# Kernel optimization log

Hardware: AMD Instinct MI355X
Metric: run time of the kernel (lower is better)

## Reference

```python
import jax, jax.numpy as jnp
import numpy as np

SIGMA = 1.0
EPS = 1e-8  # torch nn.CosineSimilarity eps


def setup_inputs() -> dict:
    key = jax.random.key(0)
    kx, ky = jax.random.split(key)
    ex = jax.random.normal(kx, (8192, 768), dtype=jnp.float32)
    ey = jax.random.normal(ky, (16384, 768), dtype=jnp.float32)
    return {"ex": ex, "ey": ey}


def _halfnormal_log_prob(v, sigma):
    # HalfNormal(sigma).log_prob(v) = 0.5*log(2/pi) - log(sigma) - v^2/(2 sigma^2)
    logc = 0.5 * jnp.log(jnp.asarray(2.0 / np.pi, v.dtype)) - jnp.log(jnp.asarray(sigma, v.dtype))
    return logc - v * v / (2.0 * sigma * sigma)


def reference(ex, ey):
    Nx, Ny = ex.shape[0], ey.shape[0]
    # cosine similarity matrix [Nx, Ny]; norms clamped like torch CosineSimilarity
    nx = jnp.maximum(jnp.linalg.norm(ex, axis=-1), EPS)  # [Nx]
    ny = jnp.maximum(jnp.linalg.norm(ey, axis=-1), EPS)  # [Ny]
    sims = jnp.einsum('nd,md->nm', ex, ey) / (nx[:, None] * ny[None, :])
    # dim = argmax([Nx, Ny]); Nx < Ny here -> reduce over axis 1 (ey side)
    dim = int(np.argmax([Nx, Ny]))
    C = sims.max(axis=dim)  # length min(Nx, Ny)
    x = 1.0 - C[:Nx]
    y = 1.0 - C[:Ny]
    lx = _halfnormal_log_prob(x, SIGMA)
    ly = _halfnormal_log_prob(y, SIGMA)
    return ((-jnp.exp(lx) * lx).sum(), (-jnp.exp(ly) * ly).sum())
```

## Files before the change

kernel.cpp:

```cpp
#include <hip/hip_runtime.h>
#include <cstdint>

#define D_DIM 768
#define BM 128
#define BN 256
#define BK 64
#define NT 12
#define ABYTES (BM * BK)
#define SLOT   (BM * BK + BN * BK)

typedef int   intx8    __attribute__((ext_vector_type(8)));
typedef float floatx16 __attribute__((ext_vector_type(16)));

#define SCALE_ONE 0x7F7F7F7F


__device__ inline void lds_load16(const void* g, void* lds) {
  __builtin_amdgcn_global_load_lds(
      (const __attribute__((address_space(1))) unsigned int*)g,
      (__attribute__((address_space(3))) unsigned int*)lds,
      16, 0, 0);
}

__device__ inline intx8 ldfrag(const unsigned char* p, int o0, int o1) {
  intx8 r;
  *(int4*)&r       = *(const int4*)(p + o0);
  *((int4*)&r + 1) = *(const int4*)(p + o1);
  return r;
}


__global__ __launch_bounds__(256) void norm_cast_kernel(
    const float* __restrict__ EX, const float* __restrict__ EY,
    unsigned int* __restrict__ XO, unsigned int* __restrict__ YO, int Nx) {
  int row = blockIdx.x * 4 + (threadIdx.x >> 6);
  int lane = threadIdx.x & 63;
  const float* X = (row < Nx) ? EX : EY;
  unsigned int* Y = (row < Nx) ? XO : YO;
  int r = (row < Nx) ? row : (row - Nx);
  const float4* xr = (const float4*)(X + (size_t)r * D_DIM);
  float4 a = xr[lane];
  float4 b = xr[lane + 64];
  float4 c = xr[lane + 128];
  float ss = a.x*a.x + a.y*a.y + a.z*a.z + a.w*a.w
           + b.x*b.x + b.y*b.y + b.z*b.z + b.w*b.w
           + c.x*c.x + c.y*c.y + c.z*c.z + c.w*c.w;
  #pragma unroll
  for (int off = 32; off > 0; off >>= 1) ss += __shfl_xor(ss, off, 64);
  float s = 1.0f / fmaxf(sqrtf(ss), 1e-8f);
  unsigned int* yr = Y + (size_t)r * (D_DIM / 4);
  int d;
  d = __builtin_amdgcn_cvt_pk_fp8_f32(a.x * s, a.y * s, 0, false);
  d = __builtin_amdgcn_cvt_pk_fp8_f32(a.z * s, a.w * s, d, true);
  yr[lane] = (unsigned int)d;
  d = __builtin_amdgcn_cvt_pk_fp8_f32(b.x * s, b.y * s, 0, false);
  d = __builtin_amdgcn_cvt_pk_fp8_f32(b.z * s, b.w * s, d, true);
  yr[lane + 64] = (unsigned int)d;
  d = __builtin_amdgcn_cvt_pk_fp8_f32(c.x * s, c.y * s, 0, false);
  d = __builtin_amdgcn_cvt_pk_fp8_f32(c.z * s, c.w * s, d, true);
  yr[lane + 128] = (unsigned int)d;
}


#define STAGE(SL, KO) do {                                                     \
    unsigned char* dst_ = lds + (SL) * SLOT;                                   \
    lds_load16(gA + (KO),            dst_ + wave * 2048);                      \
    lds_load16(gA + (KO) + g16,      dst_ + wave * 2048 + 1024);               \
    lds_load16(gB + (KO),            dst_ + ABYTES + wave * 4096);             \
    lds_load16(gB + (KO) + g16,      dst_ + ABYTES + wave * 4096 + 1024);      \
    lds_load16(gB + (KO) + 2 * g16,  dst_ + ABYTES + wave * 4096 + 2048);      \
    lds_load16(gB + (KO) + 3 * g16,  dst_ + ABYTES + wave * 4096 + 3072);      \
  } while (0)

#define MFMA(d, va, vb)                                                        \
  d = __builtin_amdgcn_mfma_scale_f32_32x32x64_f8f6f4(                         \
      va, vb, d, 0, 0, 0, SCALE_ONE, 0, SCALE_ONE)

#define COMPUTE(SL) do {                                                       \
    const unsigned char* buf_ = lds + (SL) * SLOT;                             \
    intx8 a0 = ldfrag(buf_ + arow,        o0, o1);                             \
    intx8 a1 = ldfrag(buf_ + arow + 2048, o0, o1);                             \
    intx8 b;                                                                   \
    __builtin_amdgcn_s_setprio(1);                                             \
    b = ldfrag(buf_ + brow, o0, o1);                                           \
    MFMA(acc[0][0], a0, b);                                                    \
    MFMA(acc[1][0], a1, b);                                                    \
    b = ldfrag(buf_ + brow + 2048, o0, o1);                                    \
    MFMA(acc[0][1], a0, b);                                                    \
    MFMA(acc[1][1], a1, b);                                                    \
    b = ldfrag(buf_ + brow + 4096, o0, o1);                                    \
    MFMA(acc[0][2], a0, b);                                                    \
    MFMA(acc[1][2], a1, b);                                                    \
    b = ldfrag(buf_ + brow + 6144, o0, o1);                                    \
    MFMA(acc[0][3], a0, b);                                                    \
    MFMA(acc[1][3], a1, b);                                                    \
    __builtin_amdgcn_s_setprio(0);                                             \
  } while (0)

#define WAITB(VMC) do {                                                        \
    asm volatile("s_waitcnt vmcnt(" #VMC ")" ::: "memory");                    \
    __builtin_amdgcn_s_barrier();                                              \
  } while (0)

__global__ __launch_bounds__(256, 2) void gemm_max_kernel(
    const unsigned char* __restrict__ A,
    const unsigned char* __restrict__ B,
    float* __restrict__ partial,
    int Nx) {
  __shared__ unsigned char lds[3 * SLOT];
  __shared__ float red[2][BM];

  const int tid  = threadIdx.x;
  const int wave = tid >> 6;
  const int lane = tid & 63;
  const int wm = wave >> 1;
  const int wn = wave & 1;
  const int l31 = lane & 31;
  const int h   = lane >> 5;

  const int lid    = blockIdx.y * gridDim.x + blockIdx.x;
  const int xcd    = lid & 7;
  const int idx    = lid >> 3;
  const int sgrp   = idx >> 6;
  const int within = idx & 63;
  const int bx = sgrp * 8 + (within & 7);
  const int by = xcd * 8 + (within >> 3);

  const int bm0 = bx * BM;
  const int bn0 = by * BN;

  floatx16 acc[2][4];
  #pragma unroll
  for (int mt = 0; mt < 2; ++mt)
    #pragma unroll
    for (int nt = 0; nt < 4; ++nt)
      acc[mt][nt] = (floatx16)(0.f);

  const int akey = l31 & 3;
  const int o0 = ((2 * h + 0) ^ akey) * 16;
  const int o1 = ((2 * h + 1) ^ akey) * 16;
  const int arow = (wm * 64 + l31) * 64;
  const int brow = ABYTES + (wn * 128 + l31) * 64;

  const int srow = lane >> 2;
  const int sj = (lane & 3) ^ (srow & 3);
  const unsigned char* gA = A + (size_t)(bm0 + wave * 32 + srow) * D_DIM + sj * 16;
  const unsigned char* gB = B + (size_t)(bn0 + wave * 64 + srow) * D_DIM + sj * 16;
  const size_t g16 = (size_t)16 * D_DIM;

  STAGE(0, 0);
  STAGE(1, BK);

  #pragma unroll 1
  for (int t0 = 0; t0 < 9; t0 += 3) {
    const int kb = t0 * BK;
    WAITB(6); STAGE(2, kb + 2 * BK); COMPUTE(0);
    WAITB(6); STAGE(0, kb + 3 * BK); COMPUTE(1);
    WAITB(6); STAGE(1, kb + 4 * BK); COMPUTE(2);
  }
  WAITB(6); STAGE(2, 11 * BK); COMPUTE(0);
  WAITB(6);                    COMPUTE(1);
  WAITB(0);                    COMPUTE(2);

  #pragma unroll
  for (int mt = 0; mt < 2; ++mt) {
    #pragma unroll
    for (int reg = 0; reg < 16; ++reg) {
      float v = fmaxf(fmaxf(acc[mt][0][reg], acc[mt][1][reg]),
                      fmaxf(acc[mt][2][reg], acc[mt][3][reg]));
      #pragma unroll
      for (int off = 1; off < 32; off <<= 1)
        v = fmaxf(v, __shfl_xor(v, off, 64));
      if (l31 == 0) {
        int r = wm * 64 + mt * 32 + (reg & 3) + 8 * (reg >> 2) + 4 * h;
        red[wn][r] = v;
      }
    }
  }
  __syncthreads();
  if (tid < BM) {
    float m = fmaxf(red[0][tid], red[1][tid]);
    partial[(size_t)by * Nx + bm0 + tid] = m;
  }
}


__global__ __launch_bounds__(256) void rowmax_kernel(
    const float* __restrict__ partial, float* __restrict__ bsum, int Nx, int ncb) {
  __shared__ float sdata[4];
  int r = blockIdx.x * blockDim.x + threadIdx.x;
  float m = -1e30f;
  for (int cb = 0; cb < ncb; ++cb)
    m = fmaxf(m, partial[(size_t)cb * Nx + r]);
  float x = 1.0f - m;
  const float logc = -0.22579135264472744f;
  float l = logc - 0.5f * x * x;
  float t = -__expf(l) * l;
  #pragma unroll
  for (int off = 32; off > 0; off >>= 1) t += __shfl_xor(t, off, 64);
  int wave = threadIdx.x >> 6;
  int lane = threadIdx.x & 63;
  if (lane == 0) sdata[wave] = t;
  __syncthreads();
  if (threadIdx.x == 0)
    bsum[blockIdx.x] = sdata[0] + sdata[1] + sdata[2] + sdata[3];
}


__global__ __launch_bounds__(64) void final_kernel(
    const float* __restrict__ bsum, float* __restrict__ out, int nb) {
  int lane = threadIdx.x;
  float s = (lane < nb) ? bsum[lane] : 0.f;
  #pragma unroll
  for (int off = 32; off > 0; off >>= 1) s += __shfl_xor(s, off, 64);
  if (lane == 0) { out[0] = s; out[1] = s; }
}


extern "C" void kernel_launch(void* const* d_in, const int* in_sizes, int n_in,
                              void* d_out, int out_size, void* d_ws, size_t ws_size,
                              hipStream_t stream) {
  const float* ex = (const float*)d_in[0];
  const float* ey = (const float*)d_in[1];
  const int Nx = in_sizes[0] / D_DIM;
  const int Ny = in_sizes[1] / D_DIM;
  const int ncb = Ny / BN;

  char* ws = (char*)d_ws;
  unsigned char* exn = (unsigned char*)ws;
  unsigned char* eyn = exn + (size_t)Nx * D_DIM;
  float* partial = (float*)(ws + (size_t)(Nx + Ny) * D_DIM);
  float* bsum    = partial + (size_t)ncb * Nx;

  norm_cast_kernel<<<(Nx + Ny) / 4, 256, 0, stream>>>(
      ex, ey, (unsigned int*)exn, (unsigned int*)eyn, Nx);
  gemm_max_kernel<<<dim3(Nx / BM, Ny / BN), 256, 0, stream>>>(exn, eyn, partial, Nx);
  rowmax_kernel<<<Nx / 256, 256, 0, stream>>>(partial, bsum, Nx, ncb);
  final_kernel<<<1, 64, 0, stream>>>(bsum, (float*)d_out, Nx / 256);
}
```

Measured before the change: 280.8 us.

## Switch GEMM to double-buffered LDS with new swizzle and fuse final reduction

The GEMM main loop moves from a three-slot LDS ring with explicit vmcnt waits and s_setprio hints to a two-slot ping-pong with a full __syncthreads per stage. It also uses a new XOR swizzle for LDS staging and fragment reads, and a 1D launch grid. The separate final reduction kernel is removed, and rowmax blocks atomically add their partial sums straight into the output. This cuts prefetch depth and LDS use and drops one launch. The atomics assume the output starts at zero, and the shallower pipeline may expose more memory latency.

Result: slower. 362.0 us (+28.9%).

```diff
diff --git a/kernel.cpp b/kernel.cpp
--- a/kernel.cpp
+++ b/kernel.cpp
@@ -5,9 +5,11 @@
 #define BM 128
 #define BN 256
 #define BK 64
-#define NT 12
-#define ABYTES (BM * BK)
-#define SLOT   (BM * BK + BN * BK)
+#define ASZ (BM * BK)
+#define BSZ (BN * BK)
+#define SLOT (ASZ + BSZ)
+#define NBX 64
+#define NBY 64
 
 typedef int   intx8    __attribute__((ext_vector_type(8)));
 typedef float floatx16 __attribute__((ext_vector_type(16)));
@@ -62,52 +64,48 @@
 }
 
 
-#define STAGE(SL, KO) do {                                                     \
-    unsigned char* dst_ = lds + (SL) * SLOT;                                   \
-    lds_load16(gA + (KO),            dst_ + wave * 2048);                      \
-    lds_load16(gA + (KO) + g16,      dst_ + wave * 2048 + 1024);               \
-    lds_load16(gB + (KO),            dst_ + ABYTES + wave * 4096);             \
-    lds_load16(gB + (KO) + g16,      dst_ + ABYTES + wave * 4096 + 1024);      \
-    lds_load16(gB + (KO) + 2 * g16,  dst_ + ABYTES + wave * 4096 + 2048);      \
-    lds_load16(gB + (KO) + 3 * g16,  dst_ + ABYTES + wave * 4096 + 3072);      \
+#define STAGE(P, KO) do {                                                      \
+    unsigned char* dst_ = lds + (P) * SLOT;                                    \
+    unsigned char* dA_ = dst_ + wave * 2048;                                   \
+    unsigned char* dB_ = dst_ + ASZ + wave * 4096;                             \
+    lds_load16(gA + (KO),            dA_);                                     \
+    lds_load16(gA + (KO) + g16,      dA_ + 1024);                              \
+    lds_load16(gB + (KO),            dB_);                                     \
+    lds_load16(gB + (KO) + g16,      dB_ + 1024);                              \
+    lds_load16(gB + (KO) + 2 * g16,  dB_ + 2048);                              \
+    lds_load16(gB + (KO) + 3 * g16,  dB_ + 3072);                              \
   } while (0)
 
 #define MFMA(d, va, vb)                                                        \
   d = __builtin_amdgcn_mfma_scale_f32_32x32x64_f8f6f4(                         \
       va, vb, d, 0, 0, 0, SCALE_ONE, 0, SCALE_ONE)
 
-#define COMPUTE(SL) do {                                                       \
-    const unsigned char* buf_ = lds + (SL) * SLOT;                             \
-    intx8 a0 = ldfrag(buf_ + arow,        o0, o1);                             \
-    intx8 a1 = ldfrag(buf_ + arow + 2048, o0, o1);                             \
+#define COMPUTE(P) do {                                                        \
+    const unsigned char* bA_ = lds + (P) * SLOT + wm * 4096;                   \
+    const unsigned char* bB_ = lds + (P) * SLOT + ASZ + wn * 8192;             \
+    intx8 a0 = ldfrag(bA_,        o0, o1);                                     \
+    intx8 a1 = ldfrag(bA_ + 2048, o0, o1);                                     \
     intx8 b;                                                                   \
-    __builtin_amdgcn_s_setprio(1);                                             \
-    b = ldfrag(buf_ + brow, o0, o1);                                           \
+    b = ldfrag(bB_, o0, o1);                                                   \
     MFMA(acc[0][0], a0, b);                                                    \
     MFMA(acc[1][0], a1, b);                                                    \
-    b = ldfrag(buf_ + brow + 2048, o0, o1);                                    \
+    b = ldfrag(bB_ + 2048, o0, o1);                                            \
     MFMA(acc[0][1], a0, b);                                                    \
     MFMA(acc[1][1], a1, b);                                                    \
-    b = ldfrag(buf_ + brow + 4096, o0, o1);                                    \
+    b = ldfrag(bB_ + 4096, o0, o1);                                            \
     MFMA(acc[0][2], a0, b);                                                    \
     MFMA(acc[1][2], a1, b);                                                    \
-    b = ldfrag(buf_ + brow + 6144, o0, o1);                                    \
+    b = ldfrag(bB_ + 6144, o0, o1);                                            \
     MFMA(acc[0][3], a0, b);                                                    \
     MFMA(acc[1][3], a1, b);                                                    \
-    __builtin_amdgcn_s_setprio(0);                                             \
   } while (0)
 
-#define WAITB(VMC) do {                                                        \
-    asm volatile("s_waitcnt vmcnt(" #VMC ")" ::: "memory");                    \
-    __builtin_amdgcn_s_barrier();                                              \
-  } while (0)
-
-__global__ __launch_bounds__(256, 2) void gemm_max_kernel(
+__global__ __launch_bounds__(256) void gemm_max_kernel(
     const unsigned char* __restrict__ A,
     const unsigned char* __restrict__ B,
     float* __restrict__ partial,
     int Nx) {
-  __shared__ unsigned char lds[3 * SLOT];
+  __shared__ unsigned char lds[2 * SLOT];
   __shared__ float red[2][BM];
 
   const int tid  = threadIdx.x;
@@ -118,7 +116,7 @@
   const int l31 = lane & 31;
   const int h   = lane >> 5;
 
-  const int lid    = blockIdx.y * gridDim.x + blockIdx.x;
+  const int lid    = blockIdx.x;
   const int xcd    = lid & 7;
   const int idx    = lid >> 3;
   const int sgrp   = idx >> 6;
@@ -136,31 +134,30 @@
     for (int nt = 0; nt < 4; ++nt)
       acc[mt][nt] = (floatx16)(0.f);
 
-  const int akey = l31 & 3;
-  const int o0 = ((2 * h + 0) ^ akey) * 16;
-  const int o1 = ((2 * h + 1) ^ akey) * 16;
-  const int arow = (wm * 64 + l31) * 64;
-  const int brow = ABYTES + (wn * 128 + l31) * 64;
-
-  const int srow = lane >> 2;
-  const int sj = (lane & 3) ^ (srow & 3);
-  const unsigned char* gA = A + (size_t)(bm0 + wave * 32 + srow) * D_DIM + sj * 16;
-  const unsigned char* gB = B + (size_t)(bn0 + wave * 64 + srow) * D_DIM + sj * 16;
+  const int key  = (l31 >> 1) & 7;
+  const int lrow = (l31 >> 1) * 128;
+  const int c0   = 2 * h;
+  const int o0 = lrow + ((((l31 & 1) << 2) | c0)       ^ key) * 16;
+  const int o1 = lrow + ((((l31 & 1) << 2) | (c0 + 1)) ^ key) * 16;
+
+  const int ls   = (lane & 7) ^ (lane >> 3);
+  const int srow = 2 * (lane >> 3) + (ls >> 2);
+  const int sc   = ls & 3;
+  const unsigned char* gA = A + (size_t)(bm0 + wave * 32 + srow) * D_DIM + sc * 16;
+  const unsigned char* gB = B + (size_t)(bn0 + wave * 64 + srow) * D_DIM + sc * 16;
   const size_t g16 = (size_t)16 * D_DIM;
 
   STAGE(0, 0);
-  STAGE(1, BK);
+  __syncthreads();
 
   #pragma unroll 1
-  for (int t0 = 0; t0 < 9; t0 += 3) {
-    const int kb = t0 * BK;
-    WAITB(6); STAGE(2, kb + 2 * BK); COMPUTE(0);
-    WAITB(6); STAGE(0, kb + 3 * BK); COMPUTE(1);
-    WAITB(6); STAGE(1, kb + 4 * BK); COMPUTE(2);
-  }
-  WAITB(6); STAGE(2, 11 * BK); COMPUTE(0);
-  WAITB(6);                    COMPUTE(1);
-  WAITB(0);                    COMPUTE(2);
+  for (int t2 = 0; t2 < 5; ++t2) {
+    const int kb = t2 * 2 * BK;
+    STAGE(1, kb + BK);     COMPUTE(0);  __syncthreads();
+    STAGE(0, kb + 2 * BK); COMPUTE(1);  __syncthreads();
+  }
+  STAGE(1, 11 * BK);  COMPUTE(0);  __syncthreads();
+  COMPUTE(1);
 
   #pragma unroll
   for (int mt = 0; mt < 2; ++mt) {
@@ -186,7 +183,7 @@
 
 
 __global__ __launch_bounds__(256) void rowmax_kernel(
-    const float* __restrict__ partial, float* __restrict__ bsum, int Nx, int ncb) {
+    const float* __restrict__ partial, float* __restrict__ out, int Nx, int ncb) {
   __shared__ float sdata[4];
   int r = blockIdx.x * blockDim.x + threadIdx.x;
   float m = -1e30f;
@@ -202,18 +199,11 @@
   int lane = threadIdx.x & 63;
   if (lane == 0) sdata[wave] = t;
   __syncthreads();
-  if (threadIdx.x == 0)
-    bsum[blockIdx.x] = sdata[0] + sdata[1] + sdata[2] + sdata[3];
-}
-
-
-__global__ __launch_bounds__(64) void final_kernel(
-    const float* __restrict__ bsum, float* __restrict__ out, int nb) {
-  int lane = threadIdx.x;
-  float s = (lane < nb) ? bsum[lane] : 0.f;
-  #pragma unroll
-  for (int off = 32; off > 0; off >>= 1) s += __shfl_xor(s, off, 64);
-  if (lane == 0) { out[0] = s; out[1] = s; }
+  if (threadIdx.x == 0) {
+    float s = sdata[0] + sdata[1] + sdata[2] + sdata[3];
+    atomicAdd(&out[0], s);
+    atomicAdd(&out[1], s);
+  }
 }
 
 
@@ -230,11 +220,9 @@
   unsigned char* exn = (unsigned char*)ws;
   unsigned char* eyn = exn + (size_t)Nx * D_DIM;
   float* partial = (float*)(ws + (size_t)(Nx + Ny) * D_DIM);
-  float* bsum    = partial + (size_t)ncb * Nx;
 
   norm_cast_kernel<<<(Nx + Ny) / 4, 256, 0, stream>>>(
       ex, ey, (unsigned int*)exn, (unsigned int*)eyn, Nx);
-  gemm_max_kernel<<<dim3(Nx / BM, Ny / BN), 256, 0, stream>>>(exn, eyn, partial, Nx);
-  rowmax_kernel<<<Nx / 256, 256, 0, stream>>>(partial, bsum, Nx, ncb);
-  final_kernel<<<1, 64, 0, stream>>>(bsum, (float*)d_out, Nx / 256);
-}
+  gemm_max_kernel<<<NBX * NBY, 256, 0, stream>>>(exn, eyn, partial, Nx);
+  rowmax_kernel<<<Nx / 256, 256, 0, stream>>>(partial, (float*)d_out, Nx, ncb);
+}
```
